# Kernel tuning notes

Hardware: AMD Instinct MI355X
Metric: run time of the kernel (lower is better)

Reference implementation:

```python
import math
import jax, jax.numpy as jnp
import numpy as np

EMBED, HEADS, LEVELS, POINTS = 256, 8, 4, 4
HEAD_DIM = EMBED // HEADS
SHAPES = ((100, 100), (50, 50), (25, 25), (13, 13))  # (h, w) per level
BS, NQ = 8, 900
NV = sum(h * w for h, w in SHAPES)


def _offset_bias():
    # Faithful to init_weights(): per-head rotated grid init for sampling_offsets bias.
    th = np.arange(HEADS, dtype=np.float32) * (2.0 * math.pi / HEADS)
    g = np.stack([np.cos(th), np.sin(th)], -1)
    g = g / np.abs(g).max(-1, keepdims=True)
    g = np.tile(g[:, None, None, :], (1, LEVELS, POINTS, 1))
    g = g * (np.arange(POINTS, dtype=np.float32) + 1.0)[None, None, :, None]
    return jnp.asarray(g.reshape(-1))


def setup_inputs() -> dict:
    key = jax.random.key(0)
    ks = jax.random.split(key, 10)
    s = 0.05
    return {
        "query": jax.random.normal(ks[0], (BS, NQ, EMBED), jnp.float32),
        "value": jax.random.normal(ks[1], (BS, NV, EMBED), jnp.float32),
        "reference_points": jax.random.uniform(ks[2], (BS, NQ, LEVELS, 2), jnp.float32),
        "spatial_shapes": jnp.array(SHAPES, jnp.int32),
        "W_off": jax.random.normal(ks[3], (EMBED, HEADS * LEVELS * POINTS * 2), jnp.float32) * s,
        "b_off": _offset_bias(),
        "W_attn": jax.random.normal(ks[4], (EMBED, HEADS * LEVELS * POINTS), jnp.float32) * s,
        "b_attn": jnp.zeros((HEADS * LEVELS * POINTS,), jnp.float32),
        "W_v": jax.random.normal(ks[5], (EMBED, EMBED), jnp.float32) * s,
        "b_v": jnp.zeros((EMBED,), jnp.float32),
        "W_out": jax.random.normal(ks[6], (EMBED, EMBED), jnp.float32) * s,
        "b_out": jnp.zeros((EMBED,), jnp.float32),
    }


def _bilinear_sample(vl, loc, H, W, aw):
    """grid_sample bilinear, align_corners=False, zero padding, fused with attn weights.

    vl:  (bs, heads, H*W, d)   loc: (bs, nq, heads, P, 2) in [0,1] (x, y)
    aw:  (bs, heads, nq, P)    ->   (bs, heads, nq, d)
    """
    x = loc[..., 0] * W - 0.5
    y = loc[..., 1] * H - 0.5
    x0 = jnp.floor(x)
    y0 = jnp.floor(y)
    lx = x - x0
    ly = y - y0
    x0i = x0.astype(jnp.int32)
    y0i = y0.astype(jnp.int32)
    bs, heads = vl.shape[0], vl.shape[1]
    nq, P = loc.shape[1], loc.shape[3]
    acc = jnp.zeros((bs, heads, nq, vl.shape[-1]), vl.dtype)
    corners = ((0, 0, (1 - lx) * (1 - ly)), (1, 0, lx * (1 - ly)),
               (0, 1, (1 - lx) * ly), (1, 1, lx * ly))
    for dx, dy, wgt in corners:
        xi = x0i + dx
        yi = y0i + dy
        valid = ((xi >= 0) & (xi < W) & (yi >= 0) & (yi < H)).astype(vl.dtype)
        idx = jnp.clip(yi, 0, H - 1) * W + jnp.clip(xi, 0, W - 1)  # (bs, nq, heads, P)
        idx = idx.transpose(0, 2, 1, 3).reshape(bs, heads, nq * P)
        g = jnp.take_along_axis(vl, idx[..., None], axis=2).reshape(bs, heads, nq, P, -1)
        cw = (wgt * valid).transpose(0, 2, 1, 3) * aw  # (bs, heads, nq, P)
        acc = acc + (g * cw[..., None]).sum(3)
    return acc


def reference(query, value, reference_points, spatial_shapes,
              W_off, b_off, W_attn, b_attn, W_v, b_v, W_out, b_out):
    identity = query
    bs, nq, _ = query.shape
    v = (value @ W_v + b_v).reshape(bs, -1, HEADS, HEAD_DIM)
    off = (query @ W_off + b_off).reshape(bs, nq, HEADS, LEVELS, POINTS, 2)
    aw = (query @ W_attn + b_attn).reshape(bs, nq, HEADS, LEVELS * POINTS)
    aw = jax.nn.softmax(aw, -1).reshape(bs, nq, HEADS, LEVELS, POINTS)
    # offset normalizer is (w, h) per level
    norm = jnp.stack([spatial_shapes[:, 1], spatial_shapes[:, 0]], -1).astype(query.dtype)
    loc = reference_points[:, :, None, :, None, :] + off / norm[None, None, None, :, None, :]
    sizes = [h * w for h, w in SHAPES]
    starts = np.cumsum([0] + sizes[:-1])
    out = jnp.zeros((bs, HEADS, nq, HEAD_DIM), query.dtype)
    for l, (h, w) in enumerate(SHAPES):
        vl = jax.lax.dynamic_slice_in_dim(v, int(starts[l]), sizes[l], axis=1)
        vl = vl.transpose(0, 2, 1, 3)  # (bs, heads, h*w, d)
        aw_l = aw[:, :, :, l].transpose(0, 2, 1, 3)  # (bs, heads, nq, P)
        out = out + _bilinear_sample(vl, loc[:, :, :, l], h, w, aw_l)
    out = out.transpose(0, 2, 1, 3).reshape(bs, nq, EMBED)
    return out @ W_out + b_out + identity
```

## Files before the change

### kernel.cpp

```cpp
#include <hip/hip_runtime.h>
#include <hip/hip_bf16.h>

#define EMBED    256
#define HEADS    8
#define LEVELS   4
#define POINTS   4
#define HEAD_DIM 32
#define BS       8
#define NQ       900
#define NV       13294
#define MV       (BS*NV)
#define MQ       (BS*NQ)
#define NQOUT    384

typedef float  f32x4  __attribute__((ext_vector_type(4)));
typedef __bf16 bf16x8 __attribute__((ext_vector_type(8)));
typedef unsigned short ushort8 __attribute__((ext_vector_type(8)));

__device__ __forceinline__ unsigned short f2bf(float f) {
    unsigned u = __builtin_bit_cast(unsigned, f);
    u += 0x7FFFu + ((u >> 16) & 1u);
    return (unsigned short)(u >> 16);
}
__device__ __forceinline__ float bf2f(unsigned short h) {
    unsigned u = ((unsigned)h) << 16;
    return __builtin_bit_cast(float, u);
}

__global__ __launch_bounds__(256) void prep_kernel(
    const float* __restrict__ Wv,  const float* __restrict__ Woff,
    const float* __restrict__ Wattn, const float* __restrict__ Wout,
    const float* __restrict__ boff, const float* __restrict__ battn,
    unsigned short* __restrict__ WtV, unsigned short* __restrict__ WtQ,
    unsigned short* __restrict__ WtO, float* __restrict__ biasQ)
{
    int n = blockIdx.x;
    int k = threadIdx.x;
    if (n < 256) {
        WtV[n * 256 + k] = f2bf(Wv [k * 256 + n]);
        WtO[n * 256 + k] = f2bf(Wout[k * 256 + n]);
        WtQ[n * 256 + k] = f2bf(Woff[k * 256 + n]);
    } else {
        int j = n - 256;
        WtQ[n * 256 + k] = f2bf(Wattn[k * 128 + j]);
    }
    if (k == 0) biasQ[n] = (n < 256) ? boff[n] : battn[n - 256];
}

template <int WGM, int WGN, bool OUT_BF16, bool ADD_ID>
__global__ __launch_bounds__(256) void gemm_kernel(
    const float* __restrict__ A, const unsigned short* __restrict__ Bt,
    const float* __restrict__ bias, const float* __restrict__ Ident,
    void* __restrict__ C, int M, int K, int Ntot)
{
    constexpr int BM = WGM * 64, BN = WGN * 64, BK = 32;
    constexpr int LDK = 40;
    __shared__ unsigned short As[BM * LDK];
    __shared__ unsigned short Bs[BN * LDK];

    const int tid  = threadIdx.x;
    const int wave = tid >> 6, lane = tid & 63;
    const int wm = wave / WGN, wn = wave % WGN;
    const int m0 = blockIdx.x * BM;
    const int n0 = blockIdx.y * BN;
    const int lrow = lane & 15;
    const int kq   = lane >> 4;

    f32x4 acc[4][4] = {};

    for (int kk = 0; kk < K; kk += BK) {
        #pragma unroll
        for (int c = 0; c < (BM * BK) / (256 * 8); ++c) {
            int flat = (c * 256 + tid) * 8;
            int row = flat >> 5, k0 = flat & 31;
            int gr = m0 + row;
            ushort8 w;
            if (gr < M) {
                const float* src = A + (size_t)gr * K + kk + k0;
                f32x4 v0 = *(const f32x4*)(src);
                f32x4 v1 = *(const f32x4*)(src + 4);
                #pragma unroll
                for (int e = 0; e < 4; ++e) { w[e] = f2bf(v0[e]); w[4+e] = f2bf(v1[e]); }
            } else {
                w = (ushort8)0;
            }
            *(ushort8*)&As[row * LDK + k0] = w;
        }
        #pragma unroll
        for (int c = 0; c < (BN * BK) / (256 * 8); ++c) {
            int flat = (c * 256 + tid) * 8;
            int row = flat >> 5, k0 = flat & 31;
            ushort8 w = *(const ushort8*)(Bt + (size_t)(n0 + row) * K + kk + k0);
            *(ushort8*)&Bs[row * LDK + k0] = w;
        }
        __syncthreads();

        bf16x8 afrag[4], bfrag[4];
        #pragma unroll
        for (int i = 0; i < 4; ++i)
            afrag[i] = *(const bf16x8*)&As[(wm * 64 + i * 16 + lrow) * LDK + kq * 8];
        #pragma unroll
        for (int j = 0; j < 4; ++j)
            bfrag[j] = *(const bf16x8*)&Bs[(wn * 64 + j * 16 + lrow) * LDK + kq * 8];
        #pragma unroll
        for (int i = 0; i < 4; ++i)
            #pragma unroll
            for (int j = 0; j < 4; ++j)
                acc[i][j] = __builtin_amdgcn_mfma_f32_16x16x32_bf16(
                    afrag[i], bfrag[j], acc[i][j], 0, 0, 0);
        __syncthreads();
    }

    #pragma unroll
    for (int i = 0; i < 4; ++i) {
        #pragma unroll
        for (int j = 0; j < 4; ++j) {
            int n = n0 + wn * 64 + j * 16 + lrow;
            float bn = bias[n];
            #pragma unroll
            for (int r = 0; r < 4; ++r) {
                int m = m0 + wm * 64 + i * 16 + kq * 4 + r;
                if (m < M) {
                    float val = acc[i][j][r] + bn;
                    if (ADD_ID) val += Ident[(size_t)m * Ntot + n];
                    if (OUT_BF16)
                        ((unsigned short*)C)[(size_t)m * Ntot + n] = f2bf(val);
                    else
                        ((float*)C)[(size_t)m * Ntot + n] = val;
                }
            }
        }
    }
}

__device__ const int   LVL_W[4]  = {100, 50, 25, 13};
__device__ const int   LVL_H[4]  = {100, 50, 25, 13};
__device__ const int   LVL_S[4]  = {0, 10000, 12500, 13125};

__global__ __launch_bounds__(256) void sample_kernel(
    const unsigned short* __restrict__ V,
    const float* __restrict__ Qout,
    const float* __restrict__ RP,
    float* __restrict__ OutS)
{
    const int gid = blockIdx.x * 16 + (threadIdx.x >> 4);
    const int s   = threadIdx.x & 15;
    const int h   = gid & 7;
    const int bq  = gid >> 3;
    const int b   = bq / NQ;

    const float* qrow = Qout + (size_t)bq * NQOUT;

    const int l = s >> 2;
    const float ox = qrow[h * 32 + 2 * s];
    const float oy = qrow[h * 32 + 2 * s + 1];
    float logit    = qrow[256 + h * 16 + s];
    const float rpx = RP[((size_t)bq * 4 + l) * 2 + 0];
    const float rpy = RP[((size_t)bq * 4 + l) * 2 + 1];
    int W = LVL_W[l], H = LVL_H[l], st = LVL_S[l];
    float x = rpx * (float)W + ox - 0.5f;
    float y = rpy * (float)H + oy - 0.5f;
    float fx = floorf(x), fy = floorf(y);
    float lx = x - fx, ly = y - fy;
    int ix = (int)fx, iy = (int)fy;

    float mx = logit;
    #pragma unroll
    for (int o = 8; o; o >>= 1) mx = fmaxf(mx, __shfl_xor(mx, o, 16));
    float e = __expf(logit - mx);
    float sum = e;
    #pragma unroll
    for (int o = 8; o; o >>= 1) sum += __shfl_xor(sum, o, 16);
    const float wgt = e / sum;

    const unsigned short* vb = V + ((size_t)b * NV) * 256 + h * 32 + 2 * s;
    float ax = 0.f, ay = 0.f;

    #pragma unroll
    for (int sp = 0; sp < 16; ++sp) {
        float ws  = __shfl(wgt, sp, 16);
        float lxs = __shfl(lx,  sp, 16);
        float lys = __shfl(ly,  sp, 16);
        int  ixs  = __shfl(ix,  sp, 16);
        int  iys  = __shfl(iy,  sp, 16);
        int  Ws   = __shfl(W,   sp, 16);
        int  Hs   = __shfl(H,   sp, 16);
        int  sts  = __shfl(st,  sp, 16);
        #pragma unroll
        for (int corner = 0; corner < 4; ++corner) {
            int dx = corner & 1, dy = corner >> 1;
            int xi = ixs + dx, yi = iys + dy;
            float cw = ws * (dx ? lxs : 1.f - lxs) * (dy ? lys : 1.f - lys);
            if (xi >= 0 && xi < Ws && yi >= 0 && yi < Hs && cw != 0.f) {
                const unsigned short* p = vb + (size_t)(sts + yi * Ws + xi) * 256;
                unsigned pv = *(const unsigned*)p;
                ax += cw * bf2f((unsigned short)(pv & 0xFFFF));
                ay += cw * bf2f((unsigned short)(pv >> 16));
            }
        }
    }
    float2* o = (float2*)(OutS + (size_t)bq * 256 + h * 32);
    o[s] = make_float2(ax, ay);
}

extern "C" void kernel_launch(void* const* d_in, const int* in_sizes, int n_in,
                              void* d_out, int out_size, void* d_ws, size_t ws_size,
                              hipStream_t stream)
{
    const float* query  = (const float*)d_in[0];
    const float* value  = (const float*)d_in[1];
    const float* rp     = (const float*)d_in[2];
    const float* W_off  = (const float*)d_in[4];
    const float* b_off  = (const float*)d_in[5];
    const float* W_attn = (const float*)d_in[6];
    const float* b_attn = (const float*)d_in[7];
    const float* W_v    = (const float*)d_in[8];
    const float* b_v    = (const float*)d_in[9];
    const float* W_out  = (const float*)d_in[10];
    const float* b_out  = (const float*)d_in[11];

    char* ws = (char*)d_ws;
    size_t off = 0;
    unsigned short* Vbf = (unsigned short*)(ws + off); off += (size_t)MV * 256 * 2;
    float* qout         = (float*)(ws + off);          off += (size_t)MQ * NQOUT * 4;
    float* outs         = (float*)(ws + off);          off += (size_t)MQ * 256 * 4;
    unsigned short* WtV = (unsigned short*)(ws + off); off += 256 * 256 * 2;
    unsigned short* WtQ = (unsigned short*)(ws + off); off += 384 * 256 * 2;
    unsigned short* WtO = (unsigned short*)(ws + off); off += 256 * 256 * 2;
    float* biasQ        = (float*)(ws + off);          off += 384 * 4;

    prep_kernel<<<384, 256, 0, stream>>>(W_v, W_off, W_attn, W_out, b_off, b_attn,
                                         WtV, WtQ, WtO, biasQ);

    gemm_kernel<1, 4, true, false><<<dim3((MV + 63) / 64, 1), 256, 0, stream>>>(
        value, WtV, b_v, nullptr, Vbf, MV, 256, 256);

    gemm_kernel<2, 2, false, false><<<dim3((MQ + 127) / 128, 3), 256, 0, stream>>>(
        query, WtQ, biasQ, nullptr, qout, MQ, 256, NQOUT);

    sample_kernel<<<(BS * NQ * HEADS) / 16, 256, 0, stream>>>(Vbf, qout, rp, outs);

    gemm_kernel<2, 2, false, true><<<dim3((MQ + 127) / 128, 2), 256, 0, stream>>>(
        outs, WtO, b_out, query, (float*)d_out, MQ, 256, 256);
}
```

Measured before the change: 318.2 us.

## Double-buffer GEMM LDS tiles with register prefetch and change LDS padding

The GEMM main loop now loads the next K-tile of A (fp32) and B (bf16) into registers while MFMAs run on the current LDS buffer. Shared memory is double-buffered, which drops one __syncthreads per iteration. The launch bound and per-thread chunking are now derived from the workgroup shape. LDS row padding goes from 40 to 34 elements, which leaves 16-byte vector LDS accesses misaligned and may add bank or alignment penalties.

```diff
diff --git a/kernel.cpp b/kernel.cpp
--- a/kernel.cpp
+++ b/kernel.cpp
@@ -48,15 +48,18 @@
 }
 
 template <int WGM, int WGN, bool OUT_BF16, bool ADD_ID>
-__global__ __launch_bounds__(256) void gemm_kernel(
+__global__ __launch_bounds__(WGM* WGN * 64) void gemm_kernel(
     const float* __restrict__ A, const unsigned short* __restrict__ Bt,
     const float* __restrict__ bias, const float* __restrict__ Ident,
     void* __restrict__ C, int M, int K, int Ntot)
 {
+    constexpr int NTHR = WGM * WGN * 64;
     constexpr int BM = WGM * 64, BN = WGN * 64, BK = 32;
-    constexpr int LDK = 40;
-    __shared__ unsigned short As[BM * LDK];
-    __shared__ unsigned short Bs[BN * LDK];
+    constexpr int LDK = 34;
+    constexpr int ACH = (BM * BK) / NTHR;
+    constexpr int BCH = (BN * BK) / NTHR;
+    __shared__ unsigned short As[2][BM * LDK];
+    __shared__ unsigned short Bs[2][BN * LDK];
 
     const int tid  = threadIdx.x;
     const int wave = tid >> 6, lane = tid & 63;
@@ -66,49 +69,73 @@
     const int lrow = lane & 15;
     const int kq   = lane >> 4;
 
-    f32x4 acc[4][4] = {};
-
-    for (int kk = 0; kk < K; kk += BK) {
-        #pragma unroll
-        for (int c = 0; c < (BM * BK) / (256 * 8); ++c) {
-            int flat = (c * 256 + tid) * 8;
+    f32x4   areg[ACH / 4];
+    ushort8 breg[BCH / 8];
+    f32x4   acc[4][4] = {};
+
+    auto loadA = [&](int kk) {
+        #pragma unroll
+        for (int i = 0; i < ACH / 4; ++i) {
+            int flat = tid * ACH + i * 4;
             int row = flat >> 5, k0 = flat & 31;
             int gr = m0 + row;
+            areg[i] = (gr < M) ? *(const f32x4*)(A + (size_t)gr * K + kk + k0)
+                               : (f32x4)0.f;
+        }
+    };
+    auto loadB = [&](int kk) {
+        #pragma unroll
+        for (int i = 0; i < BCH / 8; ++i) {
+            int flat = tid * BCH + i * 8;
+            int row = flat >> 5, k0 = flat & 31;
+            breg[i] = *(const ushort8*)(Bt + (size_t)(n0 + row) * K + kk + k0);
+        }
+    };
+    auto storeA = [&](int buf) {
+        #pragma unroll
+        for (int i = 0; i < ACH / 8; ++i) {
+            int flat = tid * ACH + i * 8;
+            int row = flat >> 5, k0 = flat & 31;
             ushort8 w;
-            if (gr < M) {
-                const float* src = A + (size_t)gr * K + kk + k0;
-                f32x4 v0 = *(const f32x4*)(src);
-                f32x4 v1 = *(const f32x4*)(src + 4);
-                #pragma unroll
-                for (int e = 0; e < 4; ++e) { w[e] = f2bf(v0[e]); w[4+e] = f2bf(v1[e]); }
-            } else {
-                w = (ushort8)0;
+            #pragma unroll
+            for (int e = 0; e < 4; ++e) {
+                w[e]     = f2bf(areg[2 * i][e]);
+                w[4 + e] = f2bf(areg[2 * i + 1][e]);
             }
-            *(ushort8*)&As[row * LDK + k0] = w;
-        }
-        #pragma unroll
-        for (int c = 0; c < (BN * BK) / (256 * 8); ++c) {
-            int flat = (c * 256 + tid) * 8;
-            int row = flat >> 5, k0 = flat & 31;
-            ushort8 w = *(const ushort8*)(Bt + (size_t)(n0 + row) * K + kk + k0);
-            *(ushort8*)&Bs[row * LDK + k0] = w;
-        }
+            *(ushort8*)&As[buf][row * LDK + k0] = w;
+        }
+    };
+    auto storeB = [&](int buf) {
+        #pragma unroll
+        for (int i = 0; i < BCH / 8; ++i) {
+            int flat = tid * BCH + i * 8;
+            int row = flat >> 5, k0 = flat & 31;
+            *(ushort8*)&Bs[buf][row * LDK + k0] = breg[i];
+        }
+    };
+
+    loadA(0); loadB(0);
+    const int KT = K / BK;
+    for (int kt = 0; kt < KT; ++kt) {
+        const int buf = kt & 1;
+        storeA(buf);
+        storeB(buf);
         __syncthreads();
+        if (kt + 1 < KT) { loadA((kt + 1) * BK); loadB((kt + 1) * BK); }
 
         bf16x8 afrag[4], bfrag[4];
         #pragma unroll
         for (int i = 0; i < 4; ++i)
-            afrag[i] = *(const bf16x8*)&As[(wm * 64 + i * 16 + lrow) * LDK + kq * 8];
+            afrag[i] = *(const bf16x8*)&As[buf][(wm * 64 + i * 16 + lrow) * LDK + kq * 8];
         #pragma unroll
         for (int j = 0; j < 4; ++j)
-            bfrag[j] = *(const bf16x8*)&Bs[(wn * 64 + j * 16 + lrow) * LDK + kq * 8];
+            bfrag[j] = *(const bf16x8*)&Bs[buf][(wn * 64 + j * 16 + lrow) * LDK + kq * 8];
         #pragma unroll
         for (int i = 0; i < 4; ++i)
             #pragma unroll
             for (int j = 0; j < 4; ++j)
                 acc[i][j] = __builtin_amdgcn_mfma_f32_16x16x32_bf16(
                     afrag[i], bfrag[j], acc[i][j], 0, 0, 0);
-        __syncthreads();
     }
 
     #pragma unroll
```

Measured after the change: 322.0 us. About the same (+1.2%).

## Replace tiled GEMMs with persistent weight-resident streaming GEMM kernels

Applied to the files above, without the earlier changes.

Replaces the K-looped shared-memory tiled GEMM with a persistent kernel that loads the whole bf16 weight slice (all K=256) into LDS once per block. Each wave then streams 16-row strips of the fp32 activations straight from global memory into registers, converts them to bf16 and runs MFMAs against the resident weights, with vectorized epilogue stores. This removes repeated weight tile loads and per-K-step barriers and uses a grid-stride loop over rows. In exchange it needs large LDS and many registers per wave, and it assumes M is a multiple of 16 with no tail handling.

```diff
diff --git a/kernel.cpp b/kernel.cpp
--- a/kernel.cpp
+++ b/kernel.cpp
@@ -15,7 +15,8 @@
 
 typedef float  f32x4  __attribute__((ext_vector_type(4)));
 typedef __bf16 bf16x8 __attribute__((ext_vector_type(8)));
-typedef unsigned short ushort8 __attribute__((ext_vector_type(8)));
+typedef unsigned short ushort8  __attribute__((ext_vector_type(8)));
+typedef unsigned short ushort4v __attribute__((ext_vector_type(4)));
 
 __device__ __forceinline__ unsigned short f2bf(float f) {
     unsigned u = __builtin_bit_cast(unsigned, f);
@@ -47,87 +48,77 @@
     if (k == 0) biasQ[n] = (n < 256) ? boff[n] : battn[n - 256];
 }
 
-template <int WGM, int WGN, bool OUT_BF16, bool ADD_ID>
-__global__ __launch_bounds__(256) void gemm_kernel(
-    const float* __restrict__ A, const unsigned short* __restrict__ Bt,
-    const float* __restrict__ bias, const float* __restrict__ Ident,
-    void* __restrict__ C, int M, int K, int Ntot)
-{
-    constexpr int BM = WGM * 64, BN = WGN * 64, BK = 32;
-    constexpr int LDK = 40;
-    __shared__ unsigned short As[BM * LDK];
-    __shared__ unsigned short Bs[BN * LDK];
-
-    const int tid  = threadIdx.x;
+#define LDKB 264
+
+template <int NT, bool OUT_BF16, bool ADD_ID>
+__global__ __launch_bounds__(512, 2) void gemm_stream(
+    const float* __restrict__ A,
+    const unsigned short* __restrict__ BtBase,
+    const float* __restrict__ biasBase,
+    const float* __restrict__ Ident,
+    void* __restrict__ Cv, int Ntot, int M)
+{
+    const int n0 = blockIdx.y * (NT * 16);
+    const unsigned short* Bt = BtBase + (size_t)n0 * 256;
+    const float* bias = biasBase + n0;
+
+    __shared__ unsigned short Bs[NT * 16 * LDKB];
+    const int tid = threadIdx.x;
+    #pragma unroll
+    for (int i = 0; i < NT; ++i) {
+        int flat = (i * 512 + tid) * 8;
+        int row = flat >> 8, k0 = flat & 255;
+        *(ushort8*)&Bs[row * LDKB + k0] = *(const ushort8*)(Bt + flat);
+    }
+    __syncthreads();
+
     const int wave = tid >> 6, lane = tid & 63;
-    const int wm = wave / WGN, wn = wave % WGN;
-    const int m0 = blockIdx.x * BM;
-    const int n0 = blockIdx.y * BN;
-    const int lrow = lane & 15;
-    const int kq   = lane >> 4;
-
-    f32x4 acc[4][4] = {};
-
-    for (int kk = 0; kk < K; kk += BK) {
-        #pragma unroll
-        for (int c = 0; c < (BM * BK) / (256 * 8); ++c) {
-            int flat = (c * 256 + tid) * 8;
-            int row = flat >> 5, k0 = flat & 31;
-            int gr = m0 + row;
-            ushort8 w;
-            if (gr < M) {
-                const float* src = A + (size_t)gr * K + kk + k0;
-                f32x4 v0 = *(const f32x4*)(src);
-                f32x4 v1 = *(const f32x4*)(src + 4);
+    const int lrow = lane & 15, kq = lane >> 4;
+    const int stride = gridDim.x * 8;
+    const int NS = M / 16;
+
+    for (int s = blockIdx.x * 8 + wave; s < NS; s += stride) {
+        const int m0 = s * 16;
+        const float* abase = A + (size_t)(m0 + lrow) * 256 + kq * 8;
+        f32x4 areg[16];
+        #pragma unroll
+        for (int c = 0; c < 8; ++c) {
+            areg[2 * c]     = *(const f32x4*)(abase + c * 32);
+            areg[2 * c + 1] = *(const f32x4*)(abase + c * 32 + 4);
+        }
+        f32x4 acc[NT];
+        #pragma unroll
+        for (int j = 0; j < NT; ++j) acc[j] = (f32x4)0.f;
+
+        #pragma unroll
+        for (int c = 0; c < 8; ++c) {
+            ushort8 vb;
+            #pragma unroll
+            for (int e = 0; e < 4; ++e) {
+                vb[e]     = f2bf(areg[2 * c][e]);
+                vb[4 + e] = f2bf(areg[2 * c + 1][e]);
+            }
+            bf16x8 vfrag = __builtin_bit_cast(bf16x8, vb);
+            #pragma unroll
+            for (int j = 0; j < NT; ++j) {
+                bf16x8 wfrag = *(const bf16x8*)&Bs[(j * 16 + lrow) * LDKB + c * 32 + kq * 8];
+                acc[j] = __builtin_amdgcn_mfma_f32_16x16x32_bf16(wfrag, vfrag, acc[j], 0, 0, 0);
+            }
+        }
+
+        const size_t crow = (size_t)(m0 + lrow) * Ntot + n0 + kq * 4;
+        #pragma unroll
+        for (int j = 0; j < NT; ++j) {
+            f32x4 r = acc[j] + *(const f32x4*)(bias + j * 16 + kq * 4);
+            if (ADD_ID)
+                r += *(const f32x4*)(Ident + (size_t)(m0 + lrow) * Ntot + n0 + j * 16 + kq * 4);
+            if (OUT_BF16) {
+                ushort4v o;
                 #pragma unroll
-                for (int e = 0; e < 4; ++e) { w[e] = f2bf(v0[e]); w[4+e] = f2bf(v1[e]); }
+                for (int e = 0; e < 4; ++e) o[e] = f2bf(r[e]);
+                *(ushort4v*)((unsigned short*)Cv + crow + j * 16) = o;
             } else {
-                w = (ushort8)0;
-            }
-            *(ushort8*)&As[row * LDK + k0] = w;
-        }
-        #pragma unroll
-        for (int c = 0; c < (BN * BK) / (256 * 8); ++c) {
-            int flat = (c * 256 + tid) * 8;
-            int row = flat >> 5, k0 = flat & 31;
-            ushort8 w = *(const ushort8*)(Bt + (size_t)(n0 + row) * K + kk + k0);
-            *(ushort8*)&Bs[row * LDK + k0] = w;
-        }
-        __syncthreads();
-
-        bf16x8 afrag[4], bfrag[4];
-        #pragma unroll
-        for (int i = 0; i < 4; ++i)
-            afrag[i] = *(const bf16x8*)&As[(wm * 64 + i * 16 + lrow) * LDK + kq * 8];
-        #pragma unroll
-        for (int j = 0; j < 4; ++j)
-            bfrag[j] = *(const bf16x8*)&Bs[(wn * 64 + j * 16 + lrow) * LDK + kq * 8];
-        #pragma unroll
-        for (int i = 0; i < 4; ++i)
-            #pragma unroll
-            for (int j = 0; j < 4; ++j)
-                acc[i][j] = __builtin_amdgcn_mfma_f32_16x16x32_bf16(
-                    afrag[i], bfrag[j], acc[i][j], 0, 0, 0);
-        __syncthreads();
-    }
-
-    #pragma unroll
-    for (int i = 0; i < 4; ++i) {
-        #pragma unroll
-        for (int j = 0; j < 4; ++j) {
-            int n = n0 + wn * 64 + j * 16 + lrow;
-            float bn = bias[n];
-            #pragma unroll
-            for (int r = 0; r < 4; ++r) {
-                int m = m0 + wm * 64 + i * 16 + kq * 4 + r;
-                if (m < M) {
-                    float val = acc[i][j][r] + bn;
-                    if (ADD_ID) val += Ident[(size_t)m * Ntot + n];
-                    if (OUT_BF16)
-                        ((unsigned short*)C)[(size_t)m * Ntot + n] = f2bf(val);
-                    else
-                        ((float*)C)[(size_t)m * Ntot + n] = val;
-                }
+                *(f32x4*)((float*)Cv + crow + j * 16) = r;
             }
         }
     }
@@ -232,14 +223,14 @@
     prep_kernel<<<384, 256, 0, stream>>>(W_v, W_off, W_attn, W_out, b_off, b_attn,
                                          WtV, WtQ, WtO, biasQ);
 
-    gemm_kernel<1, 4, true, false><<<dim3((MV + 63) / 64, 1), 256, 0, stream>>>(
-        value, WtV, b_v, nullptr, Vbf, MV, 256, 256);
-
-    gemm_kernel<2, 2, false, false><<<dim3((MQ + 127) / 128, 3), 256, 0, stream>>>(
-        query, WtQ, biasQ, nullptr, qout, MQ, 256, NQOUT);
+    gemm_stream<16, true, false><<<dim3(256, 1), 512, 0, stream>>>(
+        value, WtV, b_v, nullptr, Vbf, 256, MV);
+
+    gemm_stream<12, false, false><<<dim3(57, 2), 512, 0, stream>>>(
+        query, WtQ, biasQ, nullptr, qout, NQOUT, MQ);
 
     sample_kernel<<<(BS * NQ * HEADS) / 16, 256, 0, stream>>>(Vbf, qout, rp, outs);
 
-    gemm_kernel<2, 2, false, true><<<dim3((MQ + 127) / 128, 2), 256, 0, stream>>>(
-        outs, WtO, b_out, query, (float*)d_out, MQ, 256, 256);
-}
+    gemm_stream<16, false, true><<<dim3(57, 1), 512, 0, stream>>>(
+        outs, WtO, b_out, query, (float*)d_out, 256, MQ);
+}
```

Measured after the change: 644.8 us. 2.03x slower.
